# Kernel optimization log

Measured on AMD Instinct MI355X. Metric: run time of the kernel, lower is better.

## Reference

```python
import jax, jax.numpy as jnp
import numpy as np


def setup_inputs() -> dict:
    key = jax.random.key(0)
    ks = jax.random.split(key, 6)
    N, C, H = 3072, 2048, 16
    hd = C // H  # 128
    x = jax.random.normal(ks[0], (N, C), dtype=jnp.float32)
    # rotary frequencies as cos/sin of per-position angles (real view of complex freqs_cis)
    inv_freq = 1.0 / (10000.0 ** (np.arange(0, hd, 2, dtype=np.float32) / hd))  # [hd/2]
    angles = jnp.arange(N, dtype=jnp.float32)[:, None] * jnp.asarray(inv_freq)[None, :]  # [N, hd/2]
    freqs_cos = jnp.cos(angles)
    freqs_sin = jnp.sin(angles)
    qkv_w = jax.random.normal(ks[1], (3 * C, C), dtype=jnp.float32) * 0.02
    qkv_b = jnp.zeros((3 * C,), dtype=jnp.float32)
    proj_w = jax.random.normal(ks[2], (C, C), dtype=jnp.float32) * 0.02
    proj_b = jnp.zeros((C,), dtype=jnp.float32)
    cu_seqlens = jnp.array([0, 768, 1536, 2304, 3072], dtype=jnp.int32)
    return {
        "x": x, "freqs_cos": freqs_cos, "freqs_sin": freqs_sin,
        "qkv_w": qkv_w, "qkv_b": qkv_b, "proj_w": proj_w, "proj_b": proj_b,
        "cu_seqlens": cu_seqlens, "max_seqlen": 768,
    }


def _rope(t, cos, sin):
    # t: [H, N, hd]; interpret consecutive pairs as complex, multiply by freqs_cis
    tr, ti = t[..., 0::2], t[..., 1::2]              # [H, N, hd/2]
    o_re = tr * cos - ti * sin
    o_im = tr * sin + ti * cos
    return jnp.stack([o_re, o_im], axis=-1).reshape(t.shape)


def reference(x, freqs_cos, freqs_sin, qkv_w, qkv_b, proj_w, proj_b, cu_seqlens, max_seqlen):
    N, C = x.shape
    hd = freqs_cos.shape[-1] * 2
    H = C // hd
    qkv = (x @ qkv_w.T + qkv_b).reshape(N, 3, H, hd).transpose(1, 2, 0, 3)  # [3, H, N, hd]
    q, k, v = qkv[0], qkv[1], qkv[2]
    q = _rope(q, freqs_cos, freqs_sin)
    k = _rope(k, freqs_cos, freqs_sin)
    # varlen attention: block-diagonal mask from cu_seqlens segment membership
    seg = jnp.searchsorted(cu_seqlens[1:], jnp.arange(N), side="right")  # [N]
    mask = seg[:, None] == seg[None, :]                                  # [N, N]
    scale = 1.0 / np.sqrt(hd).astype(np.float32)
    scores = jnp.einsum("hnd,hmd->hnm", q, k) * scale                    # [H, N, N]
    scores = jnp.where(mask[None], scores, jnp.finfo(scores.dtype).min)
    probs = jax.nn.softmax(scores, axis=-1)
    out = jnp.einsum("hnm,hmd->hnd", probs, v)                           # [H, N, hd]
    out = out.transpose(1, 0, 2).reshape(N, C)
    return out @ proj_w.T + proj_b
```

## Files before the change

kernel.cpp:

```cpp
#include <hip/hip_runtime.h>
#include <stdint.h>

#define N_TOK  3072
#define C_DIM  2048
#define K3C    6144
#define NHEAD  16
#define HD     128
#define SEGLEN 768

typedef __attribute__((ext_vector_type(8))) short  short8;
typedef __attribute__((ext_vector_type(4))) float  f32x4;

__device__ __forceinline__ unsigned short f2bf(float f) {
  unsigned u = __builtin_bit_cast(unsigned, f);
  u += 0x7FFFu + ((u >> 16) & 1u);
  return (unsigned short)(u >> 16);
}
__device__ __forceinline__ float bf2f(unsigned short h) {
  unsigned u = ((unsigned)h) << 16;
  return __builtin_bit_cast(float, u);
}
__device__ __forceinline__ void gload_lds16(const void* g, void* l) {
  __builtin_amdgcn_global_load_lds(
      (const __attribute__((address_space(1))) unsigned int*)g,
      (__attribute__((address_space(3))) unsigned int*)l, 16, 0, 0);
}

#define XB_ELEMS    (3072L*2048L)
#define WQKV_ELEMS  (6144L*2048L)
#define WPROJ_ELEMS (2048L*2048L)
__global__ __launch_bounds__(256) void cast_bf16_kernel(
    const float* __restrict__ x, const float* __restrict__ wqkv,
    const float* __restrict__ wproj, unsigned short* __restrict__ xb,
    unsigned short* __restrict__ wqkvb, unsigned short* __restrict__ wprojb) {
  long t = (long)blockIdx.x * 256 + threadIdx.x;
  long i = t * 8;
  const float* src; unsigned short* dst; long off;
  if (i < XB_ELEMS)                   { src = x;     dst = xb;     off = i; }
  else if (i < XB_ELEMS + WQKV_ELEMS) { src = wqkv;  dst = wqkvb;  off = i - XB_ELEMS; }
  else                                { src = wproj; dst = wprojb; off = i - XB_ELEMS - WQKV_ELEMS; }
  f32x4 a = *(const f32x4*)(src + off);
  f32x4 b = *(const f32x4*)(src + off + 4);
  short8 o;
  #pragma unroll
  for (int k = 0; k < 4; ++k) { o[k] = (short)f2bf(a[k]); o[k+4] = (short)f2bf(b[k]); }
  *(short8*)(dst + off) = o;
}

#define VM4 asm volatile("s_waitcnt vmcnt(4)" ::: "memory");
#define VM0 asm volatile("s_waitcnt vmcnt(0)" ::: "memory");

#define STAGE_H(buf, mat, h, t, BASE) do { \
  const unsigned short* _s0 = (BASE) + (size_t)l        * (size_t)K_ \
                              + (size_t)((t)*64 + ((h)*4 + wv)*8); \
  char* _d0 = ldsB + ((((buf)*2 + (mat))*8 + (h)*4 + wv) * 128) * 16; \
  gload_lds16(_s0,                      _d0); \
  gload_lds16(_s0 + (size_t)64 * K_,    _d0 + 1024); \
} while (0)

#define PHASE4(buf, kk, STAGES, WAIT) do { \
  short8 aF[4], bF[4]; \
  _Pragma("unroll") \
  for (int m = 0; m < 4; ++m) \
    aF[m] = *(const short8*)&sH[buf][0][(kk)*4 + lh][wr*64 + m*16 + lr][0]; \
  _Pragma("unroll") \
  for (int n = 0; n < 4; ++n) \
    bF[n] = *(const short8*)&sH[buf][1][(kk)*4 + lh][wc*64 + n*16 + lr][0]; \
  STAGES \
  __builtin_amdgcn_s_barrier(); \
  asm volatile("s_waitcnt lgkmcnt(0)" ::: "memory"); \
  __builtin_amdgcn_sched_barrier(0); \
  __builtin_amdgcn_s_setprio(1); \
  _Pragma("unroll") \
  for (int m = 0; m < 4; ++m) { \
    _Pragma("unroll") \
    for (int n = 0; n < 4; ++n) \
      acc[m][n] = __builtin_amdgcn_mfma_f32_16x16x32_bf16(aF[m], bF[n], acc[m][n], 0, 0, 0); \
  } \
  __builtin_amdgcn_s_setprio(0); \
  __builtin_amdgcn_sched_barrier(0); \
  WAIT \
  __builtin_amdgcn_s_barrier(); \
} while (0)

template<bool OUTF32>
__global__ __launch_bounds__(256, 2) void gemm128(
    const unsigned short* __restrict__ A, const unsigned short* __restrict__ B,
    const float* __restrict__ bias, void* __restrict__ Cout,
    int N, int K_) {
  __shared__ __align__(16) unsigned short sH[2][2][8][128][8];
  char* ldsB = (char*)&sH[0][0][0][0][0];
  const int tid = threadIdx.x;
  const int wv = tid >> 6, l = tid & 63, lr = l & 15, lh = l >> 4;
  const int wr = wv >> 1, wc = wv & 1;
  const long row0 = (long)blockIdx.y * 128;
  const long col0 = (long)blockIdx.x * 128;
  const unsigned short* Ab = A + row0 * K_;
  const unsigned short* Bb = B + col0 * K_;
  f32x4 acc[4][4] = {};

  STAGE_H(0,0,0, 0, Ab); STAGE_H(0,1,0, 0, Bb);
  STAGE_H(0,0,1, 0, Ab); STAGE_H(0,1,1, 0, Bb);
  STAGE_H(1,0,0, 1, Ab); STAGE_H(1,1,0, 1, Bb);
  VM4
  __builtin_amdgcn_s_barrier();

  const int NITER = K_ >> 7;
  int t0 = 0;
  #pragma unroll 1
  for (int it = 0; it < NITER - 1; ++it, t0 += 2) {
    PHASE4(0, 0, STAGE_H(1,0,1, t0+1, Ab); STAGE_H(1,1,1, t0+1, Bb);, );
    PHASE4(0, 1, STAGE_H(0,0,0, t0+2, Ab); STAGE_H(0,1,0, t0+2, Bb);, VM4);
    PHASE4(1, 0, STAGE_H(0,0,1, t0+2, Ab); STAGE_H(0,1,1, t0+2, Bb);, );
    PHASE4(1, 1, STAGE_H(1,0,0, t0+3, Ab); STAGE_H(1,1,0, t0+3, Bb);, VM4);
  }
  PHASE4(0, 0, STAGE_H(1,0,1, t0+1, Ab); STAGE_H(1,1,1, t0+1, Bb);, );
  PHASE4(0, 1, , VM0);
  PHASE4(1, 0, , );
  PHASE4(1, 1, , );

  #pragma unroll
  for (int n = 0; n < 4; ++n) {
    const long col = col0 + wc*64 + n*16 + lr;
    const float bv = bias[col];
    #pragma unroll
    for (int m = 0; m < 4; ++m) {
      const long rb = row0 + wr*64 + m*16 + lh*4;
      #pragma unroll
      for (int r = 0; r < 4; ++r) {
        float val = acc[m][n][r] + bv;
        if constexpr (OUTF32) ((float*)Cout)[(rb + r)*N + col] = val;
        else ((unsigned short*)Cout)[(rb + r)*N + col] = f2bf(val);
      }
    }
  }
}

__global__ __launch_bounds__(256) void rope_kernel(
    unsigned short* __restrict__ qkv, const float* __restrict__ fcos,
    const float* __restrict__ fsin) {
  long t = (long)blockIdx.x * 256 + threadIdx.x;
  int n  = (int)(t >> 9);
  int col = (int)(t & 511) * 8;
  int j0 = (col & 127) >> 1;
  unsigned short* p = qkv + (long)n * K3C + col;
  short8 v = *(short8*)p;
  f32x4 vc = *(const f32x4*)(fcos + n*64 + j0);
  f32x4 vs = *(const f32x4*)(fsin + n*64 + j0);
  short8 o;
  #pragma unroll
  for (int i = 0; i < 4; ++i) {
    float re = bf2f((unsigned short)v[2*i]);
    float im = bf2f((unsigned short)v[2*i+1]);
    float c = vc[i], s = vs[i];
    o[2*i]   = (short)f2bf(re*c - im*s);
    o[2*i+1] = (short)f2bf(re*s + im*c);
  }
  *(short8*)p = o;
}

__global__ __launch_bounds__(256) void transpose_v_kernel(
    const unsigned short* __restrict__ qkv, unsigned short* __restrict__ vT) {
  __shared__ unsigned short sT[64*64];
  int bidx = blockIdx.x;
  const int nb = (bidx % 48) * 64; bidx /= 48;
  const int db = (bidx & 1) * 64;  bidx >>= 1;
  const int h  = bidx;
  const int tid = threadIdx.x;
  #pragma unroll
  for (int p = 0; p < 2; ++p) {
    int ch = tid + p*256;
    int row = ch >> 3, c8 = ch & 7;
    f32x4 val = *(const f32x4*)(qkv + (long)(nb + row)*K3C + 4096 + h*HD + db + c8*8);
    int off = (row*128 + c8*16) ^ ((row & 7) << 4);
    *(f32x4*)((char*)sT + off) = val;
  }
  __syncthreads();
  #pragma unroll
  for (int p = 0; p < 2; ++p) {
    int ch = tid + p*256;
    int drow = ch >> 3, nc = ch & 7;
    short8 tv;
    #pragma unroll
    for (int j = 0; j < 8; ++j) {
      int nn = nc*8 + j;
      int off = (nn*128 + drow*2) ^ ((nn & 7) << 4);
      tv[j] = *(const short*)((const char*)sT + off);
    }
    *(short8*)(vT + ((long)h*HD + db + drow)*N_TOK + nb + nc*8) = tv;
  }
}

__global__ __launch_bounds__(256) void attn_kernel(
    const unsigned short* __restrict__ qkv, const unsigned short* __restrict__ vT,
    unsigned short* __restrict__ attb) {
  __shared__ unsigned short sK [64*128];
  __shared__ unsigned short sVT[128*64];
  __shared__ unsigned short sP [4][16*72];
  const int tid = threadIdx.x;
  const int w = tid >> 6, l = tid & 63, lr = l & 15, lh = l >> 4;
  int bidx = blockIdx.x;
  const int qt = bidx % 12; bidx /= 12;
  const int h  = bidx & 15; bidx >>= 4;
  const int s  = bidx;
  const int n0 = s*SEGLEN + qt*64;
  const float scale = 0.08838834764831845f;
  const float LOG2E = 1.4426950408889634f;

  short8 aq[4];
  {
    const unsigned short* qrow = qkv + (long)(n0 + w*16 + lr)*K3C + h*HD;
    #pragma unroll
    for (int c = 0; c < 4; ++c) aq[c] = *(const short8*)(qrow + c*32 + lh*8);
  }
  f32x4 o[8] = {};
  float m_r[4] = {-1e30f, -1e30f, -1e30f, -1e30f};
  float l_r[4] = {0.f, 0.f, 0.f, 0.f};

  for (int kt = 0; kt < 12; ++kt) {
    const int kb = s*SEGLEN + kt*64;
    __syncthreads();
    #pragma unroll
    for (int p = 0; p < 4; ++p) {
      int ch = (p*4 + w)*64 + l;
      int key = ch >> 4;
      int kc  = (ch & 15) ^ (key & 7);
      gload_lds16(qkv + (long)(kb + key)*K3C + C_DIM + h*HD + kc*8,
                  (char*)sK + (size_t)(p*4 + w)*1024);
      int d   = ch >> 3;
      int kc2 = (ch & 7) ^ (d & 7);
      gload_lds16(vT + ((long)h*HD + d)*N_TOK + kb + kc2*8,
                  (char*)sVT + (size_t)(p*4 + w)*1024);
    }
    __syncthreads();

    f32x4 sacc[4] = {};
    #pragma unroll
    for (int kd = 0; kd < 4; ++kd)
      #pragma unroll
      for (int kf = 0; kf < 4; ++kf) {
        int key = kf*16 + lr;
        int off = (key*256 + kd*64 + lh*16) ^ ((key & 7) << 4);
        short8 bk = *(const short8*)((const char*)sK + off);
        sacc[kf] = __builtin_amdgcn_mfma_f32_16x16x32_bf16(aq[kd], bk, sacc[kf], 0, 0, 0);
      }

    float alpha[4];
    #pragma unroll
    for (int r = 0; r < 4; ++r) {
      float v0 = fmaxf(fmaxf(sacc[0][r], sacc[1][r]), fmaxf(sacc[2][r], sacc[3][r]));
      #pragma unroll
      for (int sh = 1; sh < 16; sh <<= 1) v0 = fmaxf(v0, __shfl_xor(v0, sh, 64));
      float pm = v0 * scale;
      float mn = fmaxf(m_r[r], pm);
      alpha[r] = __builtin_exp2f((m_r[r] - mn) * LOG2E);
      m_r[r] = mn;
    }
    float rsum[4] = {0.f, 0.f, 0.f, 0.f};
    #pragma unroll
    for (int kf = 0; kf < 4; ++kf)
      #pragma unroll
      for (int r = 0; r < 4; ++r) {
        float pv = __builtin_exp2f((sacc[kf][r]*scale - m_r[r]) * LOG2E);
        rsum[r] += pv;
        sP[w][(lh*4 + r)*72 + kf*16 + lr] = f2bf(pv);
      }
    #pragma unroll
    for (int r = 0; r < 4; ++r) {
      float t = rsum[r];
      #pragma unroll
      for (int sh = 1; sh < 16; sh <<= 1) t += __shfl_xor(t, sh, 64);
      l_r[r] = l_r[r]*alpha[r] + t;
    }
    #pragma unroll
    for (int nf = 0; nf < 8; ++nf)
      #pragma unroll
      for (int r = 0; r < 4; ++r) o[nf][r] *= alpha[r];

    #pragma unroll
    for (int ks = 0; ks < 2; ++ks) {
      short8 ap = *(const short8*)&sP[w][lr*72 + ks*32 + lh*8];
      #pragma unroll
      for (int nf = 0; nf < 8; ++nf) {
        int d = nf*16 + lr;
        int off = (d*128 + ks*64 + lh*16) ^ ((d & 7) << 4);
        short8 bv = *(const short8*)((const char*)sVT + off);
        o[nf] = __builtin_amdgcn_mfma_f32_16x16x32_bf16(ap, bv, o[nf], 0, 0, 0);
      }
    }
  }

  #pragma unroll
  for (int r = 0; r < 4; ++r) {
    float inv = 1.0f / l_r[r];
    int n = n0 + w*16 + lh*4 + r;
    unsigned short* orow = attb + (long)n*C_DIM + h*HD;
    #pragma unroll
    for (int nf = 0; nf < 8; ++nf) orow[nf*16 + lr] = f2bf(o[nf][r] * inv);
  }
}

extern "C" void kernel_launch(void* const* d_in, const int* in_sizes, int n_in,
                              void* d_out, int out_size, void* d_ws, size_t ws_size,
                              hipStream_t stream) {
  (void)in_sizes; (void)n_in; (void)out_size; (void)ws_size;
  const float* x      = (const float*)d_in[0];
  const float* fcos   = (const float*)d_in[1];
  const float* fsin   = (const float*)d_in[2];
  const float* qkv_w  = (const float*)d_in[3];
  const float* qkv_b  = (const float*)d_in[4];
  const float* proj_w = (const float*)d_in[5];
  const float* proj_b = (const float*)d_in[6];

  char* ws = (char*)d_ws;
  unsigned short* xb     = (unsigned short*)(ws + 0L);
  unsigned short* wqkvb  = (unsigned short*)(ws + 12582912L);
  unsigned short* wprojb = (unsigned short*)(ws + 37748736L);
  unsigned short* qkvb   = (unsigned short*)(ws + 46137344L);
  unsigned short* vT     = (unsigned short*)(ws + 83886080L);
  unsigned short* attb   = xb;

  cast_bf16_kernel<<<11264, 256, 0, stream>>>(x, qkv_w, proj_w, xb, wqkvb, wprojb);
  gemm128<false><<<dim3(48, 24), 256, 0, stream>>>(xb, wqkvb, qkv_b, qkvb, 6144, 2048);
  rope_kernel<<<6144, 256, 0, stream>>>(qkvb, fcos, fsin);
  transpose_v_kernel<<<1536, 256, 0, stream>>>(qkvb, vT);
  attn_kernel<<<768, 256, 0, stream>>>(qkvb, vT, attb);
  gemm128<true><<<dim3(16, 24), 256, 0, stream>>>(attb, wprojb, proj_b, d_out, 2048, 2048);
}
```

Measured before the change: 443.3 us.

## Rework GEMM into 4-stage K-32 pipeline with swizzled block order

Replaces the two-buffer K-128 GEMM pipeline with a four-slot ring of K-32 tiles, keeping three stages of async global-to-LDS loads in flight. Waves 0-1 now stage A and waves 2-3 stage B. Block IDs are remapped with an XCD-style swizzle for L2 locality, and launch bounds are raised to 3 blocks per CU. The aim is to hide memory latency better and improve cache reuse. The cost is more barriers per K step and possible register pressure under the higher occupancy target.

```diff
diff --git a/kernel.cpp b/kernel.cpp
--- a/kernel.cpp
+++ b/kernel.cpp
@@ -47,27 +47,30 @@
   *(short8*)(dst + off) = o;
 }
 
+#define VM8 asm volatile("s_waitcnt vmcnt(8)" ::: "memory");
 #define VM4 asm volatile("s_waitcnt vmcnt(4)" ::: "memory");
 #define VM0 asm volatile("s_waitcnt vmcnt(0)" ::: "memory");
 
-#define STAGE_H(buf, mat, h, t, BASE) do { \
-  const unsigned short* _s0 = (BASE) + (size_t)l        * (size_t)K_ \
-                              + (size_t)((t)*64 + ((h)*4 + wv)*8); \
-  char* _d0 = ldsB + ((((buf)*2 + (mat))*8 + (h)*4 + wv) * 128) * 16; \
-  gload_lds16(_s0,                      _d0); \
-  gload_lds16(_s0 + (size_t)64 * K_,    _d0 + 1024); \
+#define STAGE3(b, t) do { \
+  const size_t _ko = (size_t)(t)*32 + w1*16; \
+  gload_lds16(R0 + _ko,     dB + (size_t)(b)*16384);        \
+  gload_lds16(R1 + _ko,     dB + (size_t)(b)*16384 + 1024); \
+  gload_lds16(R0 + _ko + 8, dB + (size_t)(b)*16384 + 2048); \
+  gload_lds16(R1 + _ko + 8, dB + (size_t)(b)*16384 + 3072); \
 } while (0)
 
-#define PHASE4(buf, kk, STAGES, WAIT) do { \
+#define PH(b, WAIT, STAGES) do { \
+  WAIT \
+  __builtin_amdgcn_s_barrier(); \
+  __builtin_amdgcn_sched_barrier(0); \
   short8 aF[4], bF[4]; \
   _Pragma("unroll") \
   for (int m = 0; m < 4; ++m) \
-    aF[m] = *(const short8*)&sH[buf][0][(kk)*4 + lh][wr*64 + m*16 + lr][0]; \
+    aF[m] = *(const short8*)&sH[b][0][lh][wr*64 + m*16 + lr][0]; \
   _Pragma("unroll") \
   for (int n = 0; n < 4; ++n) \
-    bF[n] = *(const short8*)&sH[buf][1][(kk)*4 + lh][wc*64 + n*16 + lr][0]; \
+    bF[n] = *(const short8*)&sH[b][1][lh][wc*64 + n*16 + lr][0]; \
   STAGES \
-  __builtin_amdgcn_s_barrier(); \
   asm volatile("s_waitcnt lgkmcnt(0)" ::: "memory"); \
   __builtin_amdgcn_sched_barrier(0); \
   __builtin_amdgcn_s_setprio(1); \
@@ -79,45 +82,44 @@
   } \
   __builtin_amdgcn_s_setprio(0); \
   __builtin_amdgcn_sched_barrier(0); \
-  WAIT \
-  __builtin_amdgcn_s_barrier(); \
 } while (0)
 
 template<bool OUTF32>
-__global__ __launch_bounds__(256, 2) void gemm128(
+__global__ __launch_bounds__(256, 3) void gemmv3(
     const unsigned short* __restrict__ A, const unsigned short* __restrict__ B,
     const float* __restrict__ bias, void* __restrict__ Cout,
     int N, int K_) {
-  __shared__ __align__(16) unsigned short sH[2][2][8][128][8];
+  __shared__ __align__(16) unsigned short sH[4][2][4][128][8];
   char* ldsB = (char*)&sH[0][0][0][0][0];
   const int tid = threadIdx.x;
   const int wv = tid >> 6, l = tid & 63, lr = l & 15, lh = l >> 4;
-  const int wr = wv >> 1, wc = wv & 1;
-  const long row0 = (long)blockIdx.y * 128;
-  const long col0 = (long)blockIdx.x * 128;
-  const unsigned short* Ab = A + row0 * K_;
-  const unsigned short* Bb = B + col0 * K_;
+  const int wr = wv >> 1, wc = wv & 1, w1 = wv & 1;
+
+  const int nwg = gridDim.x * gridDim.y;
+  const int bid = blockIdx.y * gridDim.x + blockIdx.x;
+  const int swz = (bid & 7) * (nwg >> 3) + (bid >> 3);
+  const int bx = swz % gridDim.x, by = swz / gridDim.x;
+  const long row0 = (long)by * 128;
+  const long col0 = (long)bx * 128;
+
+  const unsigned short* SBase = (wv & 2) ? (B + col0 * K_) : (A + row0 * K_);
+  const unsigned short* R0 = SBase + (size_t)l * K_;
+  const unsigned short* R1 = R0 + (size_t)64 * K_;
+  char* dB = ldsB + (size_t)wv * 4096;
+
   f32x4 acc[4][4] = {};
 
-  STAGE_H(0,0,0, 0, Ab); STAGE_H(0,1,0, 0, Bb);
-  STAGE_H(0,0,1, 0, Ab); STAGE_H(0,1,1, 0, Bb);
-  STAGE_H(1,0,0, 1, Ab); STAGE_H(1,1,0, 1, Bb);
-  VM4
-  __builtin_amdgcn_s_barrier();
-
-  const int NITER = K_ >> 7;
-  int t0 = 0;
+  STAGE3(0, 0); STAGE3(1, 1); STAGE3(2, 2);
+
+  const int NT = K_ >> 5;
+  int p = 0;
   #pragma unroll 1
-  for (int it = 0; it < NITER - 1; ++it, t0 += 2) {
-    PHASE4(0, 0, STAGE_H(1,0,1, t0+1, Ab); STAGE_H(1,1,1, t0+1, Bb);, );
-    PHASE4(0, 1, STAGE_H(0,0,0, t0+2, Ab); STAGE_H(0,1,0, t0+2, Bb);, VM4);
-    PHASE4(1, 0, STAGE_H(0,0,1, t0+2, Ab); STAGE_H(0,1,1, t0+2, Bb);, );
-    PHASE4(1, 1, STAGE_H(1,0,0, t0+3, Ab); STAGE_H(1,1,0, t0+3, Bb);, VM4);
-  }
-  PHASE4(0, 0, STAGE_H(1,0,1, t0+1, Ab); STAGE_H(1,1,1, t0+1, Bb);, );
-  PHASE4(0, 1, , VM0);
-  PHASE4(1, 0, , );
-  PHASE4(1, 1, , );
+  for (; p < NT - 3; ++p) {
+    PH((p & 3), VM8, STAGE3(((p + 3) & 3), p + 3););
+  }
+  PH((p & 3), VM8, ); ++p;
+  PH((p & 3), VM4, ); ++p;
+  PH((p & 3), VM0, );
 
   #pragma unroll
   for (int n = 0; n < 4; ++n) {
@@ -321,9 +323,9 @@
   unsigned short* attb   = xb;
 
   cast_bf16_kernel<<<11264, 256, 0, stream>>>(x, qkv_w, proj_w, xb, wqkvb, wprojb);
-  gemm128<false><<<dim3(48, 24), 256, 0, stream>>>(xb, wqkvb, qkv_b, qkvb, 6144, 2048);
+  gemmv3<false><<<dim3(48, 24), 256, 0, stream>>>(xb, wqkvb, qkv_b, qkvb, 6144, 2048);
   rope_kernel<<<6144, 256, 0, stream>>>(qkvb, fcos, fsin);
   transpose_v_kernel<<<1536, 256, 0, stream>>>(qkvb, vT);
   attn_kernel<<<768, 256, 0, stream>>>(qkvb, vT, attb);
-  gemm128<true><<<dim3(16, 24), 256, 0, stream>>>(attb, wprojb, proj_b, d_out, 2048, 2048);
-}
+  gemmv3<true><<<dim3(16, 24), 256, 0, stream>>>(attb, wprojb, proj_b, d_out, 2048, 2048);
+}
```

Result: slower. 485.2 us (+9.4%).
